# Optimization experiments

Hardware: AMD Instinct MI355X
Metric: run time of the kernel (lower is better)

The kernel has to match this reference:

```python
import jax, jax.numpy as jnp
import numpy as np

N, E = 30000, 300000          # nodes, edges
IN, HID, OUT, H = 128, 256, 64, 4  # feature dims, GAT heads
NEG_SLOPE = 0.2
BN_EPS = 1e-5


def setup_inputs() -> dict:
    key = jax.random.key(0)
    ks = jax.random.split(key, 18)
    rn = lambda k, sh, sc: (jax.random.normal(k, sh, jnp.float32) * sc)
    return {
        "x": rn(ks[0], (N, IN), 1.0),
        "edge_index": jax.random.randint(ks[1], (2, E), 0, N, dtype=jnp.int64),
        # SAGEConv 1: lin_l (aggregated neighbors, with bias) + lin_r (root)
        "W1l": rn(ks[2], (IN, HID), IN ** -0.5),
        "b1l": jnp.zeros((HID,), jnp.float32),
        "W1r": rn(ks[3], (IN, HID), IN ** -0.5),
        # SAGEConv 2
        "W2l": rn(ks[4], (HID, OUT), HID ** -0.5),
        "b2l": jnp.zeros((OUT,), jnp.float32),
        "W2r": rn(ks[5], (HID, OUT), HID ** -0.5),
        # BatchNorms
        "g1": jnp.ones((HID,), jnp.float32),
        "be1": jnp.zeros((HID,), jnp.float32),
        "g2": jnp.ones((OUT,), jnp.float32),
        "be2": jnp.zeros((OUT,), jnp.float32),
        # GATConv: heads=4, concat=False (mean over heads)
        "Wg": rn(ks[6], (OUT, H * OUT), OUT ** -0.5),
        "att_src": rn(ks[7], (H, OUT), OUT ** -0.5),
        "att_dst": rn(ks[8], (H, OUT), OUT ** -0.5),
        "bg": jnp.zeros((OUT,), jnp.float32),
    }


def _forward(x, W1l, b1l, W1r, W2l, b2l, W2r, g1, be1, g2, be2,
             Wg, att_src, att_dst, bg, edge_index):
    src, dst = edge_index[0], edge_index[1]

    def sage(x, Wl, bl, Wr):
        # PyG SAGEConv: lin_l(mean_{j in N(i)} x_j) + lin_r(x_i)
        msg = jax.ops.segment_sum(x[src], dst, num_segments=N)       # [N, D]
        deg = jax.ops.segment_sum(jnp.ones((E, 1), x.dtype), dst, num_segments=N)
        agg = msg / jnp.maximum(deg, 1.0)
        return agg @ Wl + bl + x @ Wr

    def bn(x, g, b):  # batch-statistics BatchNorm1d (training-mode math)
        mu = x.mean(0)
        var = x.var(0)
        return g * (x - mu) * jax.lax.rsqrt(var + BN_EPS) + b

    x = jax.nn.relu(bn(sage(x, W1l, b1l, W1r), g1, be1))   # [N, HID]
    x = jax.nn.relu(bn(sage(x, W2l, b2l, W2r), g2, be2))   # [N, OUT]

    # GATConv with default add_self_loops=True
    loop = jnp.arange(N, dtype=src.dtype)
    s2 = jnp.concatenate([src, loop])
    d2 = jnp.concatenate([dst, loop])
    xp = (x @ Wg).reshape(N, H, OUT)                       # [N, H, D]
    a_src = (xp * att_src).sum(-1)                         # [N, H]
    a_dst = (xp * att_dst).sum(-1)                         # [N, H]
    e = jax.nn.leaky_relu(a_src[s2] + a_dst[d2], NEG_SLOPE)  # [E+N, H]
    # segment softmax over incoming edges per target node
    m = jax.ops.segment_max(e, d2, num_segments=N)
    ee = jnp.exp(e - m[d2])
    denom = jax.ops.segment_sum(ee, d2, num_segments=N)
    alpha = ee / denom[d2]                                 # [E+N, H]
    out = jax.ops.segment_sum(alpha[:, :, None] * xp[s2], d2, num_segments=N)
    out = out.mean(axis=1) + bg                            # concat=False -> head mean
    out = jax.nn.relu(out)
    return out.mean(axis=0, keepdims=True)                 # [1, OUT]


def reference(x, edge_index, W1l, b1l, W1r, W2l, b2l, W2r,
              g1, be1, g2, be2, Wg, att_src, att_dst, bg):
    return _forward(x, W1l, b1l, W1r, W2l, b2l, W2r, g1, be1, g2, be2,
                    Wg, att_src, att_dst, bg, edge_index)
```

## Files before the change

kernel.cpp:

```cpp
#include <hip/hip_runtime.h>
#include <stdint.h>

#define N_NODES 30000
#define N_EDGES 300000
#define BN_EPS  1e-5f
#define NEG_SLOPE 0.2f

typedef __attribute__((ext_vector_type(8))) short          s16x8;
typedef __attribute__((ext_vector_type(8))) unsigned short u16x8;
typedef __attribute__((ext_vector_type(4))) float          f32x4;

__device__ __forceinline__ float b2f(unsigned int u) { return __uint_as_float(u << 16); }
__device__ __forceinline__ unsigned short f2b(float f) {
    unsigned int u = __float_as_uint(f);
    return (unsigned short)((u + 0x7fffu + ((u >> 16) & 1u)) >> 16);
}
__device__ __forceinline__ unsigned int f2q(float f) {
    unsigned int s = (__float_as_uint(f) >> 31) << 7;
    float af = fminf(fabsf(f), 448.f);
    if (af < 0.015625f) {
        int m = (int)rintf(af * 512.f);
        return s | (unsigned int)m;
    }
    unsigned int b = __float_as_uint(af);
    b += 0x7FFFFu + ((b >> 20) & 1u);
    unsigned int e = (b >> 23) - 120u;
    unsigned int m = (b >> 20) & 7u;
    if (e > 15u) { e = 15u; m = 6u; }
    return s | (e << 3) | m;
}
__device__ __forceinline__ float q2f(unsigned int u) {
    unsigned int em = u & 0x7f;
    float nrm = __uint_as_float((((em >> 3) + 120u) << 23) | ((em & 7u) << 20));
    float den = (float)em * 0.001953125f;
    float mag = (em >= 8u) ? nrm : den;
    return (u & 0x80u) ? -mag : mag;
}
__device__ __forceinline__ float lrelu(float a) { return fmaxf(a, NEG_SLOPE * a); }

__global__ void k_prep(int* __restrict__ cnt, float* __restrict__ stats, float* __restrict__ outz,
                       const float* __restrict__ x, unsigned short* __restrict__ xb,
                       unsigned char* __restrict__ xq,
                       const float* __restrict__ W1l, const float* __restrict__ W1r,
                       const float* __restrict__ W2l, const float* __restrict__ W2r,
                       const float* __restrict__ Wg,
                       unsigned short* __restrict__ t1l, unsigned short* __restrict__ t1r,
                       unsigned short* __restrict__ t2l, unsigned short* __restrict__ t2r,
                       unsigned short* __restrict__ btf,
                       const float* __restrict__ att_src, const float* __restrict__ att_dst,
                       float* __restrict__ vsrc, float* __restrict__ vdst) {
    int b = blockIdx.x, tid = threadIdx.x;
    if (b < 118) {
        int i = b * 256 + tid;
        if (i < N_NODES) cnt[i] = 0;
        if (i < 1856) stats[i] = 0.f;
        if (b == 0 && tid < 64) outz[tid] = 0.f;
    } else if (b < 1118) {
        for (int i = (b - 118) * 256 + tid; i < N_NODES * 128 / 4; i += 256000) {
            float4 v = ((const float4*)x)[i];
            unsigned int lo = f2b(v.x) | ((unsigned int)f2b(v.y) << 16);
            unsigned int hi = f2b(v.z) | ((unsigned int)f2b(v.w) << 16);
            ((uint2*)xb)[i] = make_uint2(lo, hi);
            unsigned int q = f2q(v.x) | (f2q(v.y) << 8) | (f2q(v.z) << 16) | (f2q(v.w) << 24);
            ((unsigned int*)xq)[i] = q;
        }
    } else if (b < 1566) {
        int i = (b - 1118) * 256 + tid;
        if (i >= 114688) return;
        if (i >= 98304) {
            int j = i - 98304;
            int n = j >> 8, r = j & 255;
            int h = r >> 6, k = r & 63;
            btf[j] = f2b(Wg[k * 256 + h * 64 + n] * 0.25f);
            return;
        }
        const float* S; unsigned short* D; int K, NN, off;
        if (i < 32768)      { S = W1l; D = t1l; K = 128; NN = 256; off = 0; }
        else if (i < 65536) { S = W1r; D = t1r; K = 128; NN = 256; off = 32768; }
        else if (i < 81920) { S = W2l; D = t2l; K = 256; NN = 64;  off = 65536; }
        else                { S = W2r; D = t2r; K = 256; NN = 64;  off = 81920; }
        int j = i - off;
        int k = j / NN, n = j % NN;
        D[n * K + k] = f2b(S[j]);
    } else {
        int h = tid >> 6, k = tid & 63;
        float s = 0.f, d = 0.f;
        for (int dd = 0; dd < 64; ++dd) {
            float w = Wg[k * 256 + h * 64 + dd];
            s += w * att_src[h * 64 + dd];
            d += w * att_dst[h * 64 + dd];
        }
        vsrc[h * 64 + k] = s;
        vdst[h * 64 + k] = d;
    }
}

__global__ void k_count(const int* __restrict__ dst, int* __restrict__ cnt) {
    int e = blockIdx.x * 256 + threadIdx.x;
    if (e < N_EDGES) atomicAdd(&cnt[dst[e]], 1);
}

__global__ void k_scan1(const int* __restrict__ cnt, int* __restrict__ rowptr, int* __restrict__ bsums) {
    __shared__ int s[256];
    int tid = threadIdx.x;
    int idx = blockIdx.x * 256 + tid;
    int val = (idx < N_NODES) ? cnt[idx] : 0;
    s[tid] = val; __syncthreads();
    for (int o = 1; o < 256; o <<= 1) {
        int add = (tid >= o) ? s[tid - o] : 0;
        __syncthreads();
        s[tid] += add;
        __syncthreads();
    }
    if (idx < N_NODES) rowptr[idx] = s[tid] - val;
    if (tid == 255) bsums[blockIdx.x] = s[255];
}

__global__ void k_scan3(int* __restrict__ rowptr, const int* __restrict__ bsums, int* __restrict__ cnt) {
    __shared__ int ls[128];
    int tid = threadIdx.x;
    if (tid < 128) ls[tid] = (tid < 118) ? bsums[tid] : 0;
    __syncthreads();
    for (int o = 1; o < 128; o <<= 1) {
        int add = (tid < 128 && tid >= o) ? ls[tid - o] : 0;
        __syncthreads();
        if (tid < 128) ls[tid] += add;
        __syncthreads();
    }
    int ex = (blockIdx.x == 0) ? 0 : ls[blockIdx.x - 1];
    int idx = blockIdx.x * 256 + tid;
    if (idx < N_NODES) { rowptr[idx] += ex; cnt[idx] = 0; }
    if (idx == 0) rowptr[N_NODES] = N_EDGES;
}

__global__ void k_fill(const int* __restrict__ srcA, const int* __restrict__ dstA,
                       const int* __restrict__ rowptr, int* __restrict__ cnt, int* __restrict__ col) {
    int e = blockIdx.x * 256 + threadIdx.x;
    if (e < N_EDGES) {
        int d = dstA[e];
        int pos = rowptr[d] + atomicAdd(&cnt[d], 1);
        col[pos] = srcA[e];
    }
}

__global__ void __launch_bounds__(256) k_sage_agg_q(const unsigned char* __restrict__ Xq,
                                                    const int* __restrict__ rowptr,
                                                    const int* __restrict__ col,
                                                    unsigned short* __restrict__ out) {
    int lane = threadIdx.x & 63;
    int i = (blockIdx.x << 2) + (threadIdx.x >> 6);
    if (i >= N_NODES) return;
    int b = rowptr[i], e = rowptr[i + 1];
    float aA0 = 0.f, aA1 = 0.f, aB0 = 0.f, aB1 = 0.f;
    int p = b;
    for (; p + 4 <= e; p += 4) {
        int j0 = __builtin_nontemporal_load(col + p);
        int j1 = __builtin_nontemporal_load(col + p + 1);
        int j2 = __builtin_nontemporal_load(col + p + 2);
        int j3 = __builtin_nontemporal_load(col + p + 3);
        unsigned int u0 = *(const unsigned short*)(Xq + (size_t)j0 * 128 + lane * 2);
        unsigned int u1 = *(const unsigned short*)(Xq + (size_t)j1 * 128 + lane * 2);
        unsigned int u2 = *(const unsigned short*)(Xq + (size_t)j2 * 128 + lane * 2);
        unsigned int u3 = *(const unsigned short*)(Xq + (size_t)j3 * 128 + lane * 2);
        aA0 += q2f(u0 & 0xffu) + q2f(u2 & 0xffu);
        aA1 += q2f(u0 >> 8)    + q2f(u2 >> 8);
        aB0 += q2f(u1 & 0xffu) + q2f(u3 & 0xffu);
        aB1 += q2f(u1 >> 8)    + q2f(u3 >> 8);
    }
    for (; p < e; ++p) {
        int j = __builtin_nontemporal_load(col + p);
        unsigned int u = *(const unsigned short*)(Xq + (size_t)j * 128 + lane * 2);
        aA0 += q2f(u & 0xffu);
        aA1 += q2f(u >> 8);
    }
    float inv = 1.f / fmaxf((float)(e - b), 1.f);
    unsigned int o = f2b((aA0 + aB0) * inv) | ((unsigned int)f2b((aA1 + aB1) * inv) << 16);
    __builtin_nontemporal_store(o, (unsigned int*)(out + (size_t)i * 128 + lane * 2));
}

template<int OUTM, bool BN_A, bool STATS>
__global__ void __launch_bounds__(256) k_mgemm(const unsigned short* __restrict__ A1,
                                               const unsigned short* __restrict__ Bt1, int K1,
                                               const unsigned short* __restrict__ A2,
                                               const unsigned short* __restrict__ Bt2, int K2,
                                               const float* __restrict__ bias,
                                               void* __restrict__ Cv,
                                               unsigned char* __restrict__ Czq,
                                               unsigned short* __restrict__ Cr2,
                                               int M, int NN,
                                               const float* __restrict__ bn_sum,
                                               const float* __restrict__ bn_sq,
                                               const float* __restrict__ bn_g,
                                               const float* __restrict__ bn_be,
                                               float* __restrict__ stS, float* __restrict__ stQ) {
    __shared__ unsigned short As[64 * 32];
    __shared__ unsigned short Bs[64 * 32];
    __shared__ float bnAl[256], bnBl[256];
    int tid = threadIdx.x;
    int w = tid >> 6, l = tid & 63;
    int mBase = blockIdx.x * 64, nBase = blockIdx.y * 64;
    f32x4 acc[4] = {};

    if constexpr (BN_A) {
        float mu = bn_sum[tid] * (1.f / N_NODES);
        float var = bn_sq[tid] * (1.f / N_NODES) - mu * mu;
        float a = bn_g[tid] * rsqrtf(var + BN_EPS);
        bnAl[tid] = a;
        bnBl[tid] = bn_be[tid] - a * mu;
        __syncthreads();
    }

    auto lds_off = [](int row, int col_bf16) -> int {
        return (row * 64 + col_bf16 * 2) ^ ((row & 7) << 4);
    };
    int srow = tid >> 2;
    int schunk = (tid & 3) << 3;
    int s_w_off = lds_off(srow, schunk);
    int kgrp = (l >> 4) << 3;
    int a_off = lds_off(w * 16 + (l & 15), kgrp);
    int b_off[4];
    #pragma unroll
    for (int c = 0; c < 4; ++c) b_off[c] = lds_off(c * 16 + (l & 15), kgrp);

    for (int pair = 0; pair < 2; ++pair) {
        const unsigned short* A  = pair ? A2 : A1;
        const unsigned short* Bt = pair ? Bt2 : Bt1;
        int K = pair ? K2 : K1;
        if (K == 0) break;
        for (int k0 = 0; k0 < K; k0 += 32) {
            u16x8 av = {};
            int arow = mBase + srow;
            if (arow < M) {
                av = *(const u16x8*)&A[(size_t)arow * K + k0 + schunk];
                if constexpr (BN_A) {
                    const float* pa = &bnAl[k0 + schunk];
                    const float* pb = &bnBl[k0 + schunk];
                    #pragma unroll
                    for (int e2 = 0; e2 < 8; ++e2) {
                        float f = fmaxf(b2f(av[e2]) * pa[e2] + pb[e2], 0.f);
                        av[e2] = f2b(f);
                    }
                }
            }
            u16x8 bv = *(const u16x8*)&Bt[(size_t)(nBase + srow) * K + k0 + schunk];
            *(u16x8*)((char*)As + s_w_off) = av;
            *(u16x8*)((char*)Bs + s_w_off) = bv;
            __syncthreads();
            s16x8 a = *(const s16x8*)((const char*)As + a_off);
            #pragma unroll
            for (int c = 0; c < 4; ++c) {
                s16x8 bfr = *(const s16x8*)((const char*)Bs + b_off[c]);
                acc[c] = __builtin_amdgcn_mfma_f32_16x16x32_bf16(a, bfr, acc[c], 0, 0, 0);
            }
            __syncthreads();
        }
    }

    float* lst = (float*)As;
    if constexpr (STATS) {
        if (tid < 128) lst[tid] = 0.f;
        __syncthreads();
    }
    int colb = l & 15;
    int rbase = (l >> 4) << 2;
    #pragma unroll
    for (int c = 0; c < 4; ++c) {
        int gcol = nBase + c * 16 + colb;
        float bi = bias ? bias[gcol] : 0.f;
        float s_ = 0.f, q_ = 0.f;
        #pragma unroll
        for (int r = 0; r < 4; ++r) {
            int grow = mBase + w * 16 + rbase + r;
            if (grow < M) {
                float v = acc[c][r] + bi;
                if constexpr (OUTM == 1) {
                    ((unsigned short*)Cv)[(size_t)grow * NN + gcol] = f2b(v);
                } else {
                    if (gcol < 64) Czq[(size_t)grow * 64 + gcol] = (unsigned char)f2q(v);
                    else           Cr2[(size_t)grow * 64 + gcol - 64] = f2b(v);
                }
                if constexpr (STATS) { s_ += v; q_ += v * v; }
            }
        }
        if constexpr (STATS) {
            s_ += __shfl_xor(s_, 16); s_ += __shfl_xor(s_, 32);
            q_ += __shfl_xor(q_, 16); q_ += __shfl_xor(q_, 32);
            if (l < 16) {
                atomicAdd(&lst[c * 16 + l], s_);
                atomicAdd(&lst[64 + c * 16 + l], q_);
            }
        }
    }
    if constexpr (STATS) {
        __syncthreads();
        if (tid < 64) {
            atomicAdd(&stS[nBase + tid], lst[tid]);
            atomicAdd(&stQ[nBase + tid], lst[64 + tid]);
        }
    }
}

__global__ void __launch_bounds__(256) k_mgemm_mean(const unsigned short* __restrict__ A,
                                                    const unsigned short* __restrict__ Bt,
                                                    const float* __restrict__ bg,
                                                    float* __restrict__ out, int M) {
    __shared__ unsigned short As[64 * 32];
    __shared__ unsigned short Bs[64 * 32];
    __shared__ float lds_cols[64];
    int tid = threadIdx.x;
    int w = tid >> 6, l = tid & 63;
    int mBase = blockIdx.x * 64;
    if (tid < 64) lds_cols[tid] = 0.f;
    f32x4 acc[4] = {};

    auto lds_off = [](int row, int col_bf16) -> int {
        return (row * 64 + col_bf16 * 2) ^ ((row & 7) << 4);
    };
    int srow = tid >> 2;
    int schunk = (tid & 3) << 3;
    int s_w_off = lds_off(srow, schunk);
    int kgrp = (l >> 4) << 3;
    int a_off = lds_off(w * 16 + (l & 15), kgrp);
    int b_off[4];
    #pragma unroll
    for (int c = 0; c < 4; ++c) b_off[c] = lds_off(c * 16 + (l & 15), kgrp);

    const int K = 256;
    for (int k0 = 0; k0 < K; k0 += 32) {
        u16x8 av = {};
        int arow = mBase + srow;
        if (arow < M) av = *(const u16x8*)&A[(size_t)arow * K + k0 + schunk];
        u16x8 bv = *(const u16x8*)&Bt[(size_t)srow * K + k0 + schunk];
        *(u16x8*)((char*)As + s_w_off) = av;
        *(u16x8*)((char*)Bs + s_w_off) = bv;
        __syncthreads();
        s16x8 a = *(const s16x8*)((const char*)As + a_off);
        #pragma unroll
        for (int c = 0; c < 4; ++c) {
            s16x8 bfr = *(const s16x8*)((const char*)Bs + b_off[c]);
            acc[c] = __builtin_amdgcn_mfma_f32_16x16x32_bf16(a, bfr, acc[c], 0, 0, 0);
        }
        __syncthreads();
    }

    int colb = l & 15;
    int rbase = (l >> 4) << 2;
    #pragma unroll
    for (int c = 0; c < 4; ++c) {
        int gcol = c * 16 + colb;
        float bi = bg[gcol];
        float sc = 0.f;
        #pragma unroll
        for (int r = 0; r < 4; ++r) {
            int grow = mBase + w * 16 + rbase + r;
            if (grow < M) sc += fmaxf(acc[c][r] + bi, 0.f);
        }
        sc += __shfl_xor(sc, 16);
        sc += __shfl_xor(sc, 32);
        if (l < 16) atomicAdd(&lds_cols[c * 16 + l], sc);
    }
    __syncthreads();
    if (tid < 64) atomicAdd(out + tid, lds_cols[tid] * (1.f / N_NODES));
}

__global__ void __launch_bounds__(256) k_sage_add(const unsigned char* __restrict__ zq,
                                                  const unsigned short* __restrict__ r2,
                                                  const int* __restrict__ rowptr,
                                                  const int* __restrict__ col,
                                                  const float* __restrict__ b2l,
                                                  unsigned short* __restrict__ h2,
                                                  float* __restrict__ stS, float* __restrict__ stQ) {
    __shared__ float ls[128];
    int tid = threadIdx.x;
    if (tid < 128) ls[tid] = 0.f;
    __syncthreads();
    int lane = tid & 63;
    int wid = tid >> 6;
    float bl = b2l[lane];
    float s_ = 0.f, q_ = 0.f;
    for (int i = blockIdx.x * 4 + wid; i < N_NODES; i += gridDim.x * 4) {
        int b = rowptr[i], e = rowptr[i + 1];
        float aA = 0.f, aB = 0.f;
        int p = b;
        for (; p + 4 <= e; p += 4) {
            int j0 = __builtin_nontemporal_load(col + p);
            int j1 = __builtin_nontemporal_load(col + p + 1);
            int j2 = __builtin_nontemporal_load(col + p + 2);
            int j3 = __builtin_nontemporal_load(col + p + 3);
            float v0 = q2f(zq[(size_t)j0 * 64 + lane]);
            float v1 = q2f(zq[(size_t)j1 * 64 + lane]);
            float v2 = q2f(zq[(size_t)j2 * 64 + lane]);
            float v3 = q2f(zq[(size_t)j3 * 64 + lane]);
            aA += v0 + v2;
            aB += v1 + v3;
        }
        for (; p < e; ++p) aA += q2f(zq[(size_t)__builtin_nontemporal_load(col + p) * 64 + lane]);
        float inv = 1.f / fmaxf((float)(e - b), 1.f);
        float v = (aA + aB) * inv + bl + b2f(__builtin_nontemporal_load(r2 + (size_t)i * 64 + lane));
        __builtin_nontemporal_store(f2b(v), &h2[(size_t)i * 64 + lane]);
        s_ += v; q_ += v * v;
    }
    atomicAdd(&ls[lane], s_);
    atomicAdd(&ls[64 + lane], q_);
    __syncthreads();
    if (tid < 64) {
        atomicAdd(&stS[tid], ls[tid]);
        atomicAdd(&stQ[tid], ls[64 + tid]);
    }
}

__global__ void __launch_bounds__(256) k_attn2(const unsigned short* __restrict__ h2,
                                               const float* __restrict__ sum2,
                                               const float* __restrict__ sq2,
                                               const float* __restrict__ g2,
                                               const float* __restrict__ be2,
                                               const float* __restrict__ vsrc,
                                               const float* __restrict__ vdst,
                                               unsigned char* __restrict__ h2q,
                                               float* __restrict__ att) {
    int tid = threadIdx.x;
    int lane = tid & 63;
    int wid = tid >> 6;
    float mu = sum2[lane] * (1.f / N_NODES);
    float var = sq2[lane] * (1.f / N_NODES) - mu * mu;
    float a2 = g2[lane] * rsqrtf(var + BN_EPS);
    float b2v = be2[lane] - a2 * mu;
    float vs0 = vsrc[lane], vs1 = vsrc[64 + lane], vs2 = vsrc[128 + lane], vs3 = vsrc[192 + lane];
    float vd0 = vdst[lane], vd1 = vdst[64 + lane], vd2 = vdst[128 + lane], vd3 = vdst[192 + lane];
    for (int i = blockIdx.x * 4 + wid; i < N_NODES; i += gridDim.x * 4) {
        float v = fmaxf(b2f(__builtin_nontemporal_load(h2 + (size_t)i * 64 + lane)) * a2 + b2v, 0.f);
        h2q[(size_t)i * 64 + lane] = (unsigned char)f2q(v);
        float s0 = v * vs0, s1 = v * vs1, s2 = v * vs2, s3 = v * vs3;
        float d0 = v * vd0, d1 = v * vd1, d2 = v * vd2, d3 = v * vd3;
        #pragma unroll
        for (int o = 32; o; o >>= 1) {
            s0 += __shfl_xor(s0, o); s1 += __shfl_xor(s1, o);
            s2 += __shfl_xor(s2, o); s3 += __shfl_xor(s3, o);
            d0 += __shfl_xor(d0, o); d1 += __shfl_xor(d1, o);
            d2 += __shfl_xor(d2, o); d3 += __shfl_xor(d3, o);
        }
        if (lane == 0) {
            float4* ap = (float4*)(att + (size_t)i * 8);
            ap[0] = make_float4(s0, s1, s2, s3);
            ap[1] = make_float4(d0, d1, d2, d3);
        }
    }
}

__global__ void __launch_bounds__(256) k_gat2(const unsigned char* __restrict__ h2q,
                                              const float* __restrict__ att,
                                              const int* __restrict__ rowptr,
                                              const int* __restrict__ col,
                                              unsigned short* __restrict__ oagg) {
    int tid = threadIdx.x;
    int lane = tid & 63;
    int gw = (blockIdx.x << 2) + (tid >> 6);
    int stride = gridDim.x << 2;
    for (int i = gw; i < N_NODES; i += stride) {
        int b = rowptr[i], e = rowptr[i + 1];
        float4 ai = *(const float4*)(att + (size_t)i * 8);
        float4 ad = *(const float4*)(att + (size_t)i * 8 + 4);
        float hv = q2f(h2q[(size_t)i * 64 + lane]);
        float w0 = __expf(lrelu(ai.x + ad.x));
        float w1 = __expf(lrelu(ai.y + ad.y));
        float w2 = __expf(lrelu(ai.z + ad.z));
        float w3 = __expf(lrelu(ai.w + ad.w));
        float s0 = w0, s1 = w1, s2 = w2, s3 = w3;
        float a0 = w0 * hv, a1 = w1 * hv, a2 = w2 * hv, a3 = w3 * hv;
        int p = b;
        for (; p + 2 <= e; p += 2) {
            int j0 = __builtin_nontemporal_load(col + p);
            int j1 = __builtin_nontemporal_load(col + p + 1);
            float4 aj0 = *(const float4*)(att + (size_t)j0 * 8);
            float4 aj1 = *(const float4*)(att + (size_t)j1 * 8);
            float hj0 = q2f(h2q[(size_t)j0 * 64 + lane]);
            float hj1 = q2f(h2q[(size_t)j1 * 64 + lane]);
            float e00 = __expf(lrelu(aj0.x + ad.x));
            float e01 = __expf(lrelu(aj0.y + ad.y));
            float e02 = __expf(lrelu(aj0.z + ad.z));
            float e03 = __expf(lrelu(aj0.w + ad.w));
            float e10 = __expf(lrelu(aj1.x + ad.x));
            float e11 = __expf(lrelu(aj1.y + ad.y));
            float e12 = __expf(lrelu(aj1.z + ad.z));
            float e13 = __expf(lrelu(aj1.w + ad.w));
            s0 += e00 + e10; a0 = fmaf(e00, hj0, fmaf(e10, hj1, a0));
            s1 += e01 + e11; a1 = fmaf(e01, hj0, fmaf(e11, hj1, a1));
            s2 += e02 + e12; a2 = fmaf(e02, hj0, fmaf(e12, hj1, a2));
            s3 += e03 + e13; a3 = fmaf(e03, hj0, fmaf(e13, hj1, a3));
        }
        if (p < e) {
            int j = __builtin_nontemporal_load(col + p);
            float4 aj = *(const float4*)(att + (size_t)j * 8);
            float hj = q2f(h2q[(size_t)j * 64 + lane]);
            float e0 = __expf(lrelu(aj.x + ad.x));
            float e1 = __expf(lrelu(aj.y + ad.y));
            float e2 = __expf(lrelu(aj.z + ad.z));
            float e3 = __expf(lrelu(aj.w + ad.w));
            s0 += e0; a0 = fmaf(e0, hj, a0);
            s1 += e1; a1 = fmaf(e1, hj, a1);
            s2 += e2; a2 = fmaf(e2, hj, a2);
            s3 += e3; a3 = fmaf(e3, hj, a3);
        }
        unsigned short* op = oagg + (size_t)i * 256 + lane;
        __builtin_nontemporal_store(f2b(a0 / s0), op);
        __builtin_nontemporal_store(f2b(a1 / s1), op + 64);
        __builtin_nontemporal_store(f2b(a2 / s2), op + 128);
        __builtin_nontemporal_store(f2b(a3 / s3), op + 192);
    }
}

extern "C" void kernel_launch(void* const* d_in, const int* in_sizes, int n_in,
                              void* d_out, int out_size, void* d_ws, size_t ws_size,
                              hipStream_t stream) {
    const float* x       = (const float*)d_in[0];
    const int*   ei      = (const int*)d_in[1];
    const float* W1l     = (const float*)d_in[2];
    const float* b1l     = (const float*)d_in[3];
    const float* W1r     = (const float*)d_in[4];
    const float* W2l     = (const float*)d_in[5];
    const float* b2l     = (const float*)d_in[6];
    const float* W2r     = (const float*)d_in[7];
    const float* g1      = (const float*)d_in[8];
    const float* be1     = (const float*)d_in[9];
    const float* g2      = (const float*)d_in[10];
    const float* be2     = (const float*)d_in[11];
    const float* Wg      = (const float*)d_in[12];
    const float* att_src = (const float*)d_in[13];
    const float* att_dst = (const float*)d_in[14];
    const float* bg      = (const float*)d_in[15];
    float* out = (float*)d_out;

    char* p = (char*)d_ws;
    auto alloc = [&](size_t bytes) -> char* {
        char* q = p;
        p += (bytes + 255) & ~(size_t)255;
        return q;
    };
    int*   cnt    = (int*)alloc((size_t)N_NODES * 4);
    float* stats  = (float*)alloc(1856 * 4);
    int*   rowptr = (int*)alloc((size_t)(N_NODES + 1) * 4);
    int*   bsums  = (int*)alloc(256 * 4);
    int*   col    = (int*)alloc((size_t)N_EDGES * 4);
    unsigned short* xb  = (unsigned short*)alloc((size_t)N_NODES * 128 * 2);
    unsigned char*  xq  = (unsigned char*)alloc((size_t)N_NODES * 128);
    unsigned short* agg1b = (unsigned short*)alloc((size_t)N_NODES * 128 * 2);
    unsigned short* h1b = (unsigned short*)alloc((size_t)N_NODES * 256 * 2);
    unsigned char*  zq  = (unsigned char*)alloc((size_t)N_NODES * 64);
    unsigned short* r2  = (unsigned short*)alloc((size_t)N_NODES * 64 * 2);
    unsigned short* h2  = (unsigned short*)alloc((size_t)N_NODES * 64 * 2);
    unsigned char*  h2q = (unsigned char*)alloc((size_t)N_NODES * 64);
    float* att  = (float*)alloc((size_t)N_NODES * 8 * 4);
    unsigned short* w1lt = (unsigned short*)alloc(128 * 256 * 2);
    unsigned short* w1rt = (unsigned short*)alloc(128 * 256 * 2);
    unsigned short* w2lt = (unsigned short*)alloc(256 * 64 * 2);
    unsigned short* w2rt = (unsigned short*)alloc(256 * 64 * 2);
    unsigned short* btf  = (unsigned short*)alloc(64 * 256 * 2);

    unsigned short* oagg = xb;

    float* sum1 = stats;        float* sq1 = stats + 256;
    float* sum2 = stats + 1024; float* sq2 = stats + 1088;
    float* vsrc = stats + 1344; float* vdst = stats + 1600;

    const int* srcA = ei;
    const int* dstA = ei + N_EDGES;

    k_prep<<<1567, 256, 0, stream>>>(cnt, stats, out, x, xb, xq, W1l, W1r, W2l, W2r, Wg,
                                     w1lt, w1rt, w2lt, w2rt, btf, att_src, att_dst, vsrc, vdst);
    k_count<<<1172, 256, 0, stream>>>(dstA, cnt);
    k_scan1<<<118, 256, 0, stream>>>(cnt, rowptr, bsums);
    k_scan3<<<118, 256, 0, stream>>>(rowptr, bsums, cnt);
    k_fill<<<1172, 256, 0, stream>>>(srcA, dstA, rowptr, cnt, col);

    k_sage_agg_q<<<7500, 256, 0, stream>>>(xq, rowptr, col, agg1b);
    k_mgemm<1, false, true><<<dim3(469, 4), 256, 0, stream>>>(
        agg1b, w1lt, 128, xb, w1rt, 128, b1l, h1b, nullptr, nullptr, N_NODES, 256,
        nullptr, nullptr, nullptr, nullptr, sum1, sq1);

    k_mgemm<2, true, false><<<dim3(469, 2), 256, 0, stream>>>(
        h1b, w2lt, 256, nullptr, nullptr, 0, nullptr, nullptr, zq, r2, N_NODES, 128,
        sum1, sq1, g1, be1, nullptr, nullptr);
    k_sage_add<<<1875, 256, 0, stream>>>(zq, r2, rowptr, col, b2l, h2, sum2, sq2);

    k_attn2<<<1875, 256, 0, stream>>>(h2, sum2, sq2, g2, be2, vsrc, vdst, h2q, att);
    k_gat2<<<2048, 256, 0, stream>>>(h2q, att, rowptr, col, oagg);
    k_mgemm_mean<<<469, 256, 0, stream>>>(oagg, btf, bg, out, N_NODES);
}
```

Measured before the change: 252.6 us.

## Split gather wavefronts across four edges with wide loads, replicate BN stat atomics

The three CSR gather kernels (SAGE layer-1 mean, SAGE layer-2 mean, GAT attention aggregation) now split each 64-lane wavefront into four 16-lane groups. Each group handles a different edge and loads 4-8 features per lane with wide vector loads, with a one-step software prefetch of the column indices. Partial sums are combined across groups with xor shuffles, and only 16 lanes write the output. BatchNorm statistic atomics are spread over four replicated accumulators chosen by block index, and the readers sum the copies back together. This aims to raise memory-level parallelism and cut atomic contention, at the cost of extra shuffles, masked zero-weight work on short rows, and a larger stats buffer.

Measured after the change: 203.6 us, median of 2. 1.24x faster.

```diff
diff --git a/kernel.cpp b/kernel.cpp
--- a/kernel.cpp
+++ b/kernel.cpp
@@ -11,9 +11,9 @@
 typedef __attribute__((ext_vector_type(4))) float          f32x4;
 
 __device__ __forceinline__ float b2f(unsigned int u) { return __uint_as_float(u << 16); }
-__device__ __forceinline__ unsigned short f2b(float f) {
+__device__ __forceinline__ unsigned int f2b(float f) {
     unsigned int u = __float_as_uint(f);
-    return (unsigned short)((u + 0x7fffu + ((u >> 16) & 1u)) >> 16);
+    return (u + 0x7fffu + ((u >> 16) & 1u)) >> 16;
 }
 __device__ __forceinline__ unsigned int f2q(float f) {
     unsigned int s = (__float_as_uint(f) >> 31) << 7;
@@ -53,13 +53,13 @@
     if (b < 118) {
         int i = b * 256 + tid;
         if (i < N_NODES) cnt[i] = 0;
-        if (i < 1856) stats[i] = 0.f;
+        if (i < 3072) stats[i] = 0.f;
         if (b == 0 && tid < 64) outz[tid] = 0.f;
     } else if (b < 1118) {
         for (int i = (b - 118) * 256 + tid; i < N_NODES * 128 / 4; i += 256000) {
             float4 v = ((const float4*)x)[i];
-            unsigned int lo = f2b(v.x) | ((unsigned int)f2b(v.y) << 16);
-            unsigned int hi = f2b(v.z) | ((unsigned int)f2b(v.w) << 16);
+            unsigned int lo = f2b(v.x) | (f2b(v.y) << 16);
+            unsigned int hi = f2b(v.z) | (f2b(v.w) << 16);
             ((uint2*)xb)[i] = make_uint2(lo, hi);
             unsigned int q = f2q(v.x) | (f2q(v.y) << 8) | (f2q(v.z) << 16) | (f2q(v.w) << 24);
             ((unsigned int*)xq)[i] = q;
@@ -150,32 +150,40 @@
     int lane = threadIdx.x & 63;
     int i = (blockIdx.x << 2) + (threadIdx.x >> 6);
     if (i >= N_NODES) return;
+    int eg = lane >> 4, fq = lane & 15;
     int b = rowptr[i], e = rowptr[i + 1];
-    float aA0 = 0.f, aA1 = 0.f, aB0 = 0.f, aB1 = 0.f;
+    float a[8] = {};
     int p = b;
-    for (; p + 4 <= e; p += 4) {
-        int j0 = __builtin_nontemporal_load(col + p);
-        int j1 = __builtin_nontemporal_load(col + p + 1);
-        int j2 = __builtin_nontemporal_load(col + p + 2);
-        int j3 = __builtin_nontemporal_load(col + p + 3);
-        unsigned int u0 = *(const unsigned short*)(Xq + (size_t)j0 * 128 + lane * 2);
-        unsigned int u1 = *(const unsigned short*)(Xq + (size_t)j1 * 128 + lane * 2);
-        unsigned int u2 = *(const unsigned short*)(Xq + (size_t)j2 * 128 + lane * 2);
-        unsigned int u3 = *(const unsigned short*)(Xq + (size_t)j3 * 128 + lane * 2);
-        aA0 += q2f(u0 & 0xffu) + q2f(u2 & 0xffu);
-        aA1 += q2f(u0 >> 8)    + q2f(u2 >> 8);
-        aB0 += q2f(u1 & 0xffu) + q2f(u3 & 0xffu);
-        aB1 += q2f(u1 >> 8)    + q2f(u3 >> 8);
-    }
-    for (; p < e; ++p) {
-        int j = __builtin_nontemporal_load(col + p);
-        unsigned int u = *(const unsigned short*)(Xq + (size_t)j * 128 + lane * 2);
-        aA0 += q2f(u & 0xffu);
-        aA1 += q2f(u >> 8);
-    }
-    float inv = 1.f / fmaxf((float)(e - b), 1.f);
-    unsigned int o = f2b((aA0 + aB0) * inv) | ((unsigned int)f2b((aA1 + aB1) * inv) << 16);
-    __builtin_nontemporal_store(o, (unsigned int*)(out + (size_t)i * 128 + lane * 2));
+    int i0 = p + eg, i1 = p + 4 + eg;
+    int j0 = (i0 < e) ? col[i0] : i; float m0 = (i0 < e) ? 1.f : 0.f;
+    int j1 = (i1 < e) ? col[i1] : i; float m1 = (i1 < e) ? 1.f : 0.f;
+    while (p < e) {
+        int i2 = p + 8 + eg, i3 = p + 12 + eg;
+        int j2 = (i2 < e) ? col[i2] : i; float m2 = (i2 < e) ? 1.f : 0.f;
+        int j3 = (i3 < e) ? col[i3] : i; float m3 = (i3 < e) ? 1.f : 0.f;
+        uint2 g0 = *(const uint2*)(Xq + (size_t)j0 * 128 + fq * 8);
+        uint2 g1 = *(const uint2*)(Xq + (size_t)j1 * 128 + fq * 8);
+        #pragma unroll
+        for (int q = 0; q < 4; ++q) {
+            a[q]     += m0 * q2f((g0.x >> (q * 8)) & 0xffu) + m1 * q2f((g1.x >> (q * 8)) & 0xffu);
+            a[4 + q] += m0 * q2f((g0.y >> (q * 8)) & 0xffu) + m1 * q2f((g1.y >> (q * 8)) & 0xffu);
+        }
+        j0 = j2; m0 = m2; j1 = j3; m1 = m3; p += 8;
+    }
+    #pragma unroll
+    for (int q = 0; q < 8; ++q) {
+        a[q] += __shfl_xor(a[q], 16);
+        a[q] += __shfl_xor(a[q], 32);
+    }
+    if (lane < 16) {
+        float inv = 1.f / fmaxf((float)(e - b), 1.f);
+        uint4 o;
+        o.x = f2b(a[0] * inv) | (f2b(a[1] * inv) << 16);
+        o.y = f2b(a[2] * inv) | (f2b(a[3] * inv) << 16);
+        o.z = f2b(a[4] * inv) | (f2b(a[5] * inv) << 16);
+        o.w = f2b(a[6] * inv) | (f2b(a[7] * inv) << 16);
+        *(uint4*)(out + (size_t)i * 128 + fq * 8) = o;
+    }
 }
 
 template<int OUTM, bool BN_A, bool STATS>
@@ -202,8 +210,10 @@
     f32x4 acc[4] = {};
 
     if constexpr (BN_A) {
-        float mu = bn_sum[tid] * (1.f / N_NODES);
-        float var = bn_sq[tid] * (1.f / N_NODES) - mu * mu;
+        float su = bn_sum[tid] + bn_sum[256 + tid] + bn_sum[512 + tid] + bn_sum[768 + tid];
+        float sq = bn_sq[tid] + bn_sq[256 + tid] + bn_sq[512 + tid] + bn_sq[768 + tid];
+        float mu = su * (1.f / N_NODES);
+        float var = sq * (1.f / N_NODES) - mu * mu;
         float a = bn_g[tid] * rsqrtf(var + BN_EPS);
         bnAl[tid] = a;
         bnBl[tid] = bn_be[tid] - a * mu;
@@ -238,7 +248,7 @@
                     #pragma unroll
                     for (int e2 = 0; e2 < 8; ++e2) {
                         float f = fmaxf(b2f(av[e2]) * pa[e2] + pb[e2], 0.f);
-                        av[e2] = f2b(f);
+                        av[e2] = (unsigned short)f2b(f);
                     }
                 }
             }
@@ -274,10 +284,10 @@
             if (grow < M) {
                 float v = acc[c][r] + bi;
                 if constexpr (OUTM == 1) {
-                    ((unsigned short*)Cv)[(size_t)grow * NN + gcol] = f2b(v);
+                    ((unsigned short*)Cv)[(size_t)grow * NN + gcol] = (unsigned short)f2b(v);
                 } else {
                     if (gcol < 64) Czq[(size_t)grow * 64 + gcol] = (unsigned char)f2q(v);
-                    else           Cr2[(size_t)grow * 64 + gcol - 64] = f2b(v);
+                    else           Cr2[(size_t)grow * 64 + gcol - 64] = (unsigned short)f2b(v);
                 }
                 if constexpr (STATS) { s_ += v; q_ += v * v; }
             }
@@ -293,9 +303,10 @@
     }
     if constexpr (STATS) {
         __syncthreads();
+        int rep = (blockIdx.x & 3) * 256;
         if (tid < 64) {
-            atomicAdd(&stS[nBase + tid], lst[tid]);
-            atomicAdd(&stQ[nBase + tid], lst[64 + tid]);
+            atomicAdd(&stS[rep + nBase + tid], lst[tid]);
+            atomicAdd(&stQ[rep + nBase + tid], lst[64 + tid]);
         }
     }
 }
@@ -376,36 +387,61 @@
     __syncthreads();
     int lane = tid & 63;
     int wid = tid >> 6;
-    float bl = b2l[lane];
-    float s_ = 0.f, q_ = 0.f;
+    int eg = lane >> 4, fq = lane & 15;
+    float4 blv = ((const float4*)b2l)[fq];
+    float sa[4] = {}, qa[4] = {};
     for (int i = blockIdx.x * 4 + wid; i < N_NODES; i += gridDim.x * 4) {
         int b = rowptr[i], e = rowptr[i + 1];
-        float aA = 0.f, aB = 0.f;
+        float a[4] = {};
         int p = b;
-        for (; p + 4 <= e; p += 4) {
-            int j0 = __builtin_nontemporal_load(col + p);
-            int j1 = __builtin_nontemporal_load(col + p + 1);
-            int j2 = __builtin_nontemporal_load(col + p + 2);
-            int j3 = __builtin_nontemporal_load(col + p + 3);
-            float v0 = q2f(zq[(size_t)j0 * 64 + lane]);
-            float v1 = q2f(zq[(size_t)j1 * 64 + lane]);
-            float v2 = q2f(zq[(size_t)j2 * 64 + lane]);
-            float v3 = q2f(zq[(size_t)j3 * 64 + lane]);
-            aA += v0 + v2;
-            aB += v1 + v3;
-        }
-        for (; p < e; ++p) aA += q2f(zq[(size_t)__builtin_nontemporal_load(col + p) * 64 + lane]);
-        float inv = 1.f / fmaxf((float)(e - b), 1.f);
-        float v = (aA + aB) * inv + bl + b2f(__builtin_nontemporal_load(r2 + (size_t)i * 64 + lane));
-        __builtin_nontemporal_store(f2b(v), &h2[(size_t)i * 64 + lane]);
-        s_ += v; q_ += v * v;
-    }
-    atomicAdd(&ls[lane], s_);
-    atomicAdd(&ls[64 + lane], q_);
+        int i0 = p + eg, i1 = p + 4 + eg;
+        int j0 = (i0 < e) ? col[i0] : i; float m0 = (i0 < e) ? 1.f : 0.f;
+        int j1 = (i1 < e) ? col[i1] : i; float m1 = (i1 < e) ? 1.f : 0.f;
+        while (p < e) {
+            int i2 = p + 8 + eg, i3 = p + 12 + eg;
+            int j2 = (i2 < e) ? col[i2] : i; float m2 = (i2 < e) ? 1.f : 0.f;
+            int j3 = (i3 < e) ? col[i3] : i; float m3 = (i3 < e) ? 1.f : 0.f;
+            unsigned int g0 = *(const unsigned int*)(zq + (size_t)j0 * 64 + fq * 4);
+            unsigned int g1 = *(const unsigned int*)(zq + (size_t)j1 * 64 + fq * 4);
+            #pragma unroll
+            for (int q = 0; q < 4; ++q)
+                a[q] += m0 * q2f((g0 >> (q * 8)) & 0xffu) + m1 * q2f((g1 >> (q * 8)) & 0xffu);
+            j0 = j2; m0 = m2; j1 = j3; m1 = m3; p += 8;
+        }
+        #pragma unroll
+        for (int q = 0; q < 4; ++q) {
+            a[q] += __shfl_xor(a[q], 16);
+            a[q] += __shfl_xor(a[q], 32);
+        }
+        if (lane < 16) {
+            float inv = 1.f / fmaxf((float)(e - b), 1.f);
+            uint2 rr = *(const uint2*)(r2 + (size_t)i * 64 + fq * 4);
+            float v0 = a[0] * inv + blv.x + b2f(rr.x & 0xffffu);
+            float v1 = a[1] * inv + blv.y + b2f(rr.x >> 16);
+            float v2 = a[2] * inv + blv.z + b2f(rr.y & 0xffffu);
+            float v3 = a[3] * inv + blv.w + b2f(rr.y >> 16);
+            uint2 o;
+            o.x = f2b(v0) | (f2b(v1) << 16);
+            o.y = f2b(v2) | (f2b(v3) << 16);
+            *(uint2*)(h2 + (size_t)i * 64 + fq * 4) = o;
+            sa[0] += v0; qa[0] += v0 * v0;
+            sa[1] += v1; qa[1] += v1 * v1;
+            sa[2] += v2; qa[2] += v2 * v2;
+            sa[3] += v3; qa[3] += v3 * v3;
+        }
+    }
+    if (lane < 16) {
+        #pragma unroll
+        for (int q = 0; q < 4; ++q) {
+            atomicAdd(&ls[fq * 4 + q], sa[q]);
+            atomicAdd(&ls[64 + fq * 4 + q], qa[q]);
+        }
+    }
     __syncthreads();
+    int rep = (blockIdx.x & 3) * 64;
     if (tid < 64) {
-        atomicAdd(&stS[tid], ls[tid]);
-        atomicAdd(&stQ[tid], ls[64 + tid]);
+        atomicAdd(&stS[rep + tid], ls[tid]);
+        atomicAdd(&stQ[rep + tid], ls[64 + tid]);
     }
 }
 
@@ -421,8 +457,10 @@
     int tid = threadIdx.x;
     int lane = tid & 63;
     int wid = tid >> 6;
-    float mu = sum2[lane] * (1.f / N_NODES);
-    float var = sq2[lane] * (1.f / N_NODES) - mu * mu;
+    float su = sum2[lane] + sum2[64 + lane] + sum2[128 + lane] + sum2[192 + lane];
+    float sq = sq2[lane] + sq2[64 + lane] + sq2[128 + lane] + sq2[192 + lane];
+    float mu = su * (1.f / N_NODES);
+    float var = sq * (1.f / N_NODES) - mu * mu;
     float a2 = g2[lane] * rsqrtf(var + BN_EPS);
     float b2v = be2[lane] - a2 * mu;
     float vs0 = vsrc[lane], vs1 = vsrc[64 + lane], vs2 = vsrc[128 + lane], vs3 = vsrc[192 + lane];
@@ -454,58 +492,84 @@
                                               unsigned short* __restrict__ oagg) {
     int tid = threadIdx.x;
     int lane = tid & 63;
+    int eg = lane >> 4, fq = lane & 15;
     int gw = (blockIdx.x << 2) + (tid >> 6);
     int stride = gridDim.x << 2;
     for (int i = gw; i < N_NODES; i += stride) {
         int b = rowptr[i], e = rowptr[i + 1];
         float4 ai = *(const float4*)(att + (size_t)i * 8);
         float4 ad = *(const float4*)(att + (size_t)i * 8 + 4);
-        float hv = q2f(h2q[(size_t)i * 64 + lane]);
-        float w0 = __expf(lrelu(ai.x + ad.x));
-        float w1 = __expf(lrelu(ai.y + ad.y));
-        float w2 = __expf(lrelu(ai.z + ad.z));
-        float w3 = __expf(lrelu(ai.w + ad.w));
-        float s0 = w0, s1 = w1, s2 = w2, s3 = w3;
-        float a0 = w0 * hv, a1 = w1 * hv, a2 = w2 * hv, a3 = w3 * hv;
+        unsigned int hvg = *(const unsigned int*)(h2q + (size_t)i * 64 + fq * 4);
+        float hv[4];
+        #pragma unroll
+        for (int q = 0; q < 4; ++q) hv[q] = q2f((hvg >> (q * 8)) & 0xffu);
+        float wself0 = __expf(lrelu(ai.x + ad.x));
+        float wself1 = __expf(lrelu(ai.y + ad.y));
+        float wself2 = __expf(lrelu(ai.z + ad.z));
+        float wself3 = __expf(lrelu(ai.w + ad.w));
+        float sg = (eg == 0) ? 1.f : 0.f;
+        float s[4] = { sg * wself0, sg * wself1, sg * wself2, sg * wself3 };
+        float acc[4][4];
+        #pragma unroll
+        for (int q = 0; q < 4; ++q) {
+            acc[0][q] = s[0] * hv[q];
+            acc[1][q] = s[1] * hv[q];
+            acc[2][q] = s[2] * hv[q];
+            acc[3][q] = s[3] * hv[q];
+        }
         int p = b;
-        for (; p + 2 <= e; p += 2) {
-            int j0 = __builtin_nontemporal_load(col + p);
-            int j1 = __builtin_nontemporal_load(col + p + 1);
-            float4 aj0 = *(const float4*)(att + (size_t)j0 * 8);
-            float4 aj1 = *(const float4*)(att + (size_t)j1 * 8);
-            float hj0 = q2f(h2q[(size_t)j0 * 64 + lane]);
-            float hj1 = q2f(h2q[(size_t)j1 * 64 + lane]);
-            float e00 = __expf(lrelu(aj0.x + ad.x));
-            float e01 = __expf(lrelu(aj0.y + ad.y));
-            float e02 = __expf(lrelu(aj0.z + ad.z));
-            float e03 = __expf(lrelu(aj0.w + ad.w));
-            float e10 = __expf(lrelu(aj1.x + ad.x));
-            float e11 = __expf(lrelu(aj1.y + ad.y));
-            float e12 = __expf(lrelu(aj1.z + ad.z));
-            float e13 = __expf(lrelu(aj1.w + ad.w));
-            s0 += e00 + e10; a0 = fmaf(e00, hj0, fmaf(e10, hj1, a0));
-            s1 += e01 + e11; a1 = fmaf(e01, hj0, fmaf(e11, hj1, a1));
-            s2 += e02 + e12; a2 = fmaf(e02, hj0, fmaf(e12, hj1, a2));
-            s3 += e03 + e13; a3 = fmaf(e03, hj0, fmaf(e13, hj1, a3));
-        }
-        if (p < e) {
-            int j = __builtin_nontemporal_load(col + p);
-            float4 aj = *(const float4*)(att + (size_t)j * 8);
-            float hj = q2f(h2q[(size_t)j * 64 + lane]);
-            float e0 = __expf(lrelu(aj.x + ad.x));
-            float e1 = __expf(lrelu(aj.y + ad.y));
-            float e2 = __expf(lrelu(aj.z + ad.z));
-            float e3 = __expf(lrelu(aj.w + ad.w));
-            s0 += e0; a0 = fmaf(e0, hj, a0);
-            s1 += e1; a1 = fmaf(e1, hj, a1);
-            s2 += e2; a2 = fmaf(e2, hj, a2);
-            s3 += e3; a3 = fmaf(e3, hj, a3);
-        }
-        unsigned short* op = oagg + (size_t)i * 256 + lane;
-        __builtin_nontemporal_store(f2b(a0 / s0), op);
-        __builtin_nontemporal_store(f2b(a1 / s1), op + 64);
-        __builtin_nontemporal_store(f2b(a2 / s2), op + 128);
-        __builtin_nontemporal_store(f2b(a3 / s3), op + 192);
+        int i0 = p + eg, i1 = p + 4 + eg;
+        int j0 = (i0 < e) ? col[i0] : i; float m0 = (i0 < e) ? 1.f : 0.f;
+        int j1 = (i1 < e) ? col[i1] : i; float m1 = (i1 < e) ? 1.f : 0.f;
+        while (p < e) {
+            int i2 = p + 8 + eg, i3 = p + 12 + eg;
+            int j2 = (i2 < e) ? col[i2] : i; float m2 = (i2 < e) ? 1.f : 0.f;
+            int j3 = (i3 < e) ? col[i3] : i; float m3 = (i3 < e) ? 1.f : 0.f;
+            float4 ap0 = *(const float4*)(att + (size_t)j0 * 8);
+            float4 ap1 = *(const float4*)(att + (size_t)j1 * 8);
+            unsigned int g0 = *(const unsigned int*)(h2q + (size_t)j0 * 64 + fq * 4);
+            unsigned int g1 = *(const unsigned int*)(h2q + (size_t)j1 * 64 + fq * 4);
+            float w00 = m0 * __expf(lrelu(ap0.x + ad.x));
+            float w01 = m0 * __expf(lrelu(ap0.y + ad.y));
+            float w02 = m0 * __expf(lrelu(ap0.z + ad.z));
+            float w03 = m0 * __expf(lrelu(ap0.w + ad.w));
+            float w10 = m1 * __expf(lrelu(ap1.x + ad.x));
+            float w11 = m1 * __expf(lrelu(ap1.y + ad.y));
+            float w12 = m1 * __expf(lrelu(ap1.z + ad.z));
+            float w13 = m1 * __expf(lrelu(ap1.w + ad.w));
+            s[0] += w00 + w10; s[1] += w01 + w11; s[2] += w02 + w12; s[3] += w03 + w13;
+            #pragma unroll
+            for (int q = 0; q < 4; ++q) {
+                float x0 = q2f((g0 >> (q * 8)) & 0xffu);
+                float x1 = q2f((g1 >> (q * 8)) & 0xffu);
+                acc[0][q] = fmaf(w00, x0, fmaf(w10, x1, acc[0][q]));
+                acc[1][q] = fmaf(w01, x0, fmaf(w11, x1, acc[1][q]));
+                acc[2][q] = fmaf(w02, x0, fmaf(w12, x1, acc[2][q]));
+                acc[3][q] = fmaf(w03, x0, fmaf(w13, x1, acc[3][q]));
+            }
+            j0 = j2; m0 = m2; j1 = j3; m1 = m3; p += 8;
+        }
+        #pragma unroll
+        for (int h = 0; h < 4; ++h) {
+            s[h] += __shfl_xor(s[h], 16);
+            s[h] += __shfl_xor(s[h], 32);
+            #pragma unroll
+            for (int q = 0; q < 4; ++q) {
+                acc[h][q] += __shfl_xor(acc[h][q], 16);
+                acc[h][q] += __shfl_xor(acc[h][q], 32);
+            }
+        }
+        if (lane < 16) {
+            unsigned short* op = oagg + (size_t)i * 256 + fq * 4;
+            #pragma unroll
+            for (int h = 0; h < 4; ++h) {
+                float r = 1.f / s[h];
+                uint2 o;
+                o.x = f2b(acc[h][0] * r) | (f2b(acc[h][1] * r) << 16);
+                o.y = f2b(acc[h][2] * r) | (f2b(acc[h][3] * r) << 16);
+                *(uint2*)(op + h * 64) = o;
+            }
+        }
     }
 }
 
@@ -537,7 +601,7 @@
         return q;
     };
     int*   cnt    = (int*)alloc((size_t)N_NODES * 4);
-    float* stats  = (float*)alloc(1856 * 4);
+    float* stats  = (float*)alloc(3072 * 4);
     int*   rowptr = (int*)alloc((size_t)(N_NODES + 1) * 4);
     int*   bsums  = (int*)alloc(256 * 4);
     int*   col    = (int*)alloc((size_t)N_EDGES * 4);
@@ -558,9 +622,12 @@
 
     unsigned short* oagg = xb;
 
-    float* sum1 = stats;        float* sq1 = stats + 256;
-    float* sum2 = stats + 1024; float* sq2 = stats + 1088;
-    float* vsrc = stats + 1344; float* vdst = stats + 1600;
+    float* sum1 = stats;
+    float* sq1  = stats + 1024;
+    float* sum2 = stats + 2048;
+    float* sq2  = stats + 2304;
+    float* vsrc = stats + 2560;
+    float* vdst = stats + 2816;
 
     const int* srcA = ei;
     const int* dstA = ei + N_EDGES;
```
